# Kernel optimization log

Hardware: AMD Instinct MI355X
Metric: run time of the kernel (lower is better)

## Reference

```python
import jax, jax.numpy as jnp
import numpy as np

B, L = 2, 2048
D_MODEL = 512
KERNEL = 5
DILATIONS = (1, 2, 4, 8, 1, 2, 4, 8)
HEADS = len(DILATIONS)
HEAD_W = D_MODEL // HEADS
MODE = "center"


def _dilocal_content(x_bedl, kernel, dilations, mode):
    # x_bedl: (B, E, D, L). Returns content in layout (B, L, E, H, K, D),
    # matching LCSA's dilocal + transpose(-4,-1).transpose(-4,-2).transpose(-5,-4).
    Lx = x_bedl.shape[-1]
    per_head = []
    for d in dilations:
        P = (kernel - 1) * d
        if mode == "forward":
            pads = (P, 0)
        elif mode == "backward":
            pads = (0, P)
        else:  # center
            pads = (P // 2, P - P // 2)
        padded = jnp.pad(x_bedl, ((0, 0),) * (x_bedl.ndim - 1) + (pads,))
        win = jnp.stack([padded[..., k * d:k * d + Lx] for k in range(kernel)], axis=-2)
        per_head.append(win)
    c = jnp.stack(per_head, axis=-2)  # (B, E, D, K, H, L)
    return jnp.transpose(c, (0, 5, 1, 4, 3, 2))  # (B, L, E, H, K, D)


def setup_inputs() -> dict:
    key = jax.random.key(0)
    ks = jax.random.split(key, 6)
    s_in = 1.0 / np.sqrt(D_MODEL)
    s_out = 1.0 / np.sqrt(HEADS * HEAD_W)
    x = jax.random.normal(ks[0], (B, L, D_MODEL), jnp.float32)
    q_w = jax.random.normal(ks[1], (1, HEADS, 1, HEAD_W, D_MODEL), jnp.float32) * s_in
    q_b = jnp.zeros((1, HEADS, 1, HEAD_W), jnp.float32)
    k_w = jax.random.normal(ks[2], (1, HEADS, KERNEL, HEAD_W, D_MODEL), jnp.float32) * s_in
    k_b = jnp.zeros((1, HEADS, KERNEL, HEAD_W), jnp.float32)
    v_w = jax.random.normal(ks[3], (1, HEADS, KERNEL, HEAD_W, D_MODEL), jnp.float32) * s_in
    v_b = jnp.zeros((1, HEADS, KERNEL, HEAD_W), jnp.float32)
    o_w = jax.random.normal(ks[4], (1, D_MODEL, HEADS * HEAD_W), jnp.float32) * s_out
    o_b = jnp.zeros((1, D_MODEL), jnp.float32)
    return {"x": x, "q_w": q_w, "q_b": q_b, "k_w": k_w, "k_b": k_b,
            "v_w": v_w, "v_b": v_b, "o_w": o_w, "o_b": o_b}


def reference(x, q_w, q_b, k_w, k_b, v_w, v_b, o_w, o_b) -> jnp.ndarray:
    b, l, _ = x.shape
    # ensemble=None path: unsqueeze(-3) then transpose(-2,-1) -> (B, E=1, D, L)
    t = jnp.swapaxes(x[:, None, :, :], -2, -1)
    content = _dilocal_content(t, KERNEL, DILATIONS, MODE)  # (B, L, 1, H, K, D)
    # query uses kernel_width=1 (no padding, dilation irrelevant): (B, L, 1, H, 1, D)
    query = jnp.broadcast_to(x[:, :, None, None, None, :], (b, l, 1, HEADS, 1, D_MODEL))
    # per-(head, kernel-position) projections
    q = jnp.einsum('blehkd,ehkod->blehko', query, q_w) + q_b      # (B,L,1,H,1,O)
    k = jnp.einsum('blehkd,ehkod->blehko', content, k_w) + k_b    # (B,L,1,H,K,O)
    v = jnp.einsum('blehkd,ehkod->blehko', content, v_w) + v_b    # (B,L,1,H,K,O)
    logits = jnp.einsum('blehqo,blehko->blehqk', q, k)            # (B,L,1,H,1,K)
    score = jax.nn.softmax(logits, axis=-1)
    attn = jnp.einsum('blehqk,blehko->blehqo', score, v) / jnp.sqrt(jnp.float32(HEAD_W))
    attn = attn[..., 0, :]                                        # squeeze(-2) -> (B,L,1,H,O)
    flat = attn.reshape(b, l, 1, HEADS * HEAD_W)
    out = jnp.einsum('blef,eof->bleo', flat, o_w) + o_b           # (B,L,1,D)
    # transpose(-3,-2) then squeeze ensemble -> (B, L, D)
    return out[:, :, 0, :]
```

## Files before the change

kernel.cpp:

```cpp
#include <hip/hip_runtime.h>
#include <hip/hip_bf16.h>

using bf16 = __hip_bfloat16;
typedef __attribute__((ext_vector_type(8))) short short8;
typedef __attribute__((ext_vector_type(4))) float f32x4;

__device__ __constant__ int c_dil[8] = {1, 2, 4, 8, 1, 2, 4, 8};

__device__ inline void store1(float* p, float v) { *p = v; }
__device__ inline void store1(bf16* p, float v) { *p = __float2bfloat16(v); }

__device__ inline void gload_lds16(const void* g, void* l) {
    __builtin_amdgcn_global_load_lds(
        (const __attribute__((address_space(1))) unsigned int*)g,
        (__attribute__((address_space(3))) unsigned int*)l, 16, 0, 0);
}

template <int N> __device__ inline void vwait() {
    asm volatile("s_waitcnt vmcnt(%0)" :: "n"(N) : "memory");
    __builtin_amdgcn_sched_barrier(0);
}
__device__ inline void barrier_pin() {
    __builtin_amdgcn_s_barrier();
    __builtin_amdgcn_sched_barrier(0);
}

__device__ inline unsigned short f2bf(float f) {
    const unsigned u = __float_as_uint(f);
    return (unsigned short)((u + 0x7fffu + ((u >> 16) & 1u)) >> 16);
}
__device__ inline float bf2f(unsigned short h) { return __uint_as_float(((unsigned)h) << 16); }

__device__ inline void conv_block(const float* __restrict__ src, bf16* __restrict__ dst,
                                  int ld, int mode, int idx) {
    const float4 v = *reinterpret_cast<const float4*>(src + idx);
    const int r = idx >> 9, c = idx & 511;
    bf16* d = dst + (size_t)r * ld + c;
    const float vv[4] = {v.x, v.y, v.z, v.w};
    ushort4 hi, lo;
    unsigned short* hp = &hi.x; unsigned short* lp = &lo.x;
#pragma unroll
    for (int j = 0; j < 4; ++j) {
        hp[j] = f2bf(vv[j]);
        lp[j] = f2bf(vv[j] - bf2f(hp[j]));
    }
    *reinterpret_cast<ushort4*>(d) = hi;
    if (mode == 1) *reinterpret_cast<ushort4*>(d + 512) = lo;
}

__global__ __launch_bounds__(256) void conv_all(
    const float* __restrict__ x,  const float* __restrict__ qw, const float* __restrict__ kw,
    const float* __restrict__ vw, const float* __restrict__ ow,
    const float* __restrict__ qb, const float* __restrict__ kb,
    bf16* A2, bf16* Wqk, bf16* Wv, bf16* Wo, float* bqk)
{
    const int b = blockIdx.x, t = threadIdx.x;
    if (b < 2048)       conv_block(x,  A2,                      1024, 1, (b * 256 + t) * 4);
    else if (b < 2304)  conv_block(qw, Wqk,                      512, 0, ((b - 2048) * 256 + t) * 4);
    else if (b < 3584)  conv_block(kw, Wqk + (size_t)512 * 512,  512, 0, ((b - 2304) * 256 + t) * 4);
    else if (b < 4864)  conv_block(vw, Wv,                       512, 0, ((b - 3584) * 256 + t) * 4);
    else if (b < 5120)  conv_block(ow, Wo,                       512, 0, ((b - 4864) * 256 + t) * 4);
    else { const int i = (b - 5120) * 256 + t; bqk[i] = (i < 512) ? qb[i] : kb[i - 512]; }
}

template <bool HILO>
__device__ __forceinline__ void run_gemm(
    short* smem,
    const bf16* __restrict__ A,
    const bf16* __restrict__ W,
    const float* __restrict__ bias,
    bf16* __restrict__ C, int ldc,
    int bm, int bn)
{
    constexpr int NSTEPS = 16;
    short* Ahi = smem;
    short* Alo = smem + 8192;
    short* Bs  = smem + 16384;

    const int tid = threadIdx.x, wid = tid >> 6, lane = tid & 63;

    const int sslot = (((tid & 3) ^ ((tid >> 3) & 3)) << 4);
    const char* pAh = (const char*)A + (size_t)(bm + (tid >> 2)) * 2048 + sslot;
    const char* pB0 = (const char*)W + (size_t)(bn + (tid >> 2)) * 1024 + sslot;

    auto stage = [&](int kt) {
        char* da = (char*)(Ahi + (kt & 1) * 4096);
        char* db = (char*)(Bs  + (kt & 1) * 8192);
        gload_lds16(pAh,          da + wid * 1024);
        gload_lds16(pAh + 131072, da + 4096 + wid * 1024);
        if (HILO) {
            char* dl = (char*)(Alo + (kt & 1) * 4096);
            gload_lds16(pAh + 1024,          dl + wid * 1024);
            gload_lds16(pAh + 1024 + 131072, dl + 4096 + wid * 1024);
        }
        gload_lds16(pB0,           db + wid * 1024);
        gload_lds16(pB0 + 65536,   db + 4096 + wid * 1024);
        gload_lds16(pB0 + 131072,  db + 8192 + wid * 1024);
        gload_lds16(pB0 + 196608,  db + 12288 + wid * 1024);
        pAh += 64; pB0 += 64;
    };

    f32x4 acc[4][8];
#pragma unroll
    for (int m = 0; m < 4; ++m)
#pragma unroll
        for (int n = 0; n < 8; ++n) acc[m][n] = f32x4{0.f, 0.f, 0.f, 0.f};

    const int lr16 = lane & 15;
    const int koff = (((lane >> 4) ^ ((lr16 >> 1) & 3)) << 3);
    const int wrM = wid >> 1, wcN = wid & 1;
    const int arow0 = wrM * 64 + lr16;
    const int brow0 = wcN * 128 + lr16;

    stage(0);

    for (int kt = 0; kt < NSTEPS; ++kt) {
        vwait<0>();
        barrier_pin();

        const short* ah = Ahi + (kt & 1) * 4096;
        const short* al = Alo + (kt & 1) * 4096;
        const short* bb = Bs  + (kt & 1) * 8192;
        short8 fh[4], fl[4], bw[8];
#pragma unroll
        for (int m = 0; m < 4; ++m) {
            fh[m] = *(const short8*)&ah[(arow0 + m * 16) * 32 + koff];
            if (HILO) fl[m] = *(const short8*)&al[(arow0 + m * 16) * 32 + koff];
        }
#pragma unroll
        for (int n = 0; n < 8; ++n)
            bw[n] = *(const short8*)&bb[(brow0 + n * 16) * 32 + koff];

        if (kt + 1 < NSTEPS) stage(kt + 1);

        __builtin_amdgcn_s_setprio(1);
#pragma unroll
        for (int m = 0; m < 4; ++m)
#pragma unroll
            for (int n = 0; n < 8; ++n)
                acc[m][n] = __builtin_amdgcn_mfma_f32_16x16x32_bf16(fh[m], bw[n], acc[m][n], 0, 0, 0);
        if (HILO) {
#pragma unroll
            for (int m = 0; m < 4; ++m)
#pragma unroll
                for (int n = 0; n < 8; ++n)
                    acc[m][n] = __builtin_amdgcn_mfma_f32_16x16x32_bf16(fl[m], bw[n], acc[m][n], 0, 0, 0);
        }
        __builtin_amdgcn_s_setprio(0);
    }

    const int r4 = (lane >> 4) * 4;
#pragma unroll
    for (int m = 0; m < 4; ++m) {
#pragma unroll
        for (int n = 0; n < 8; ++n) {
            const int col = bn + wcN * 128 + n * 16 + lr16;
            const float bv = bias[col];
#pragma unroll
            for (int jj = 0; jj < 4; ++jj) {
                const int row = bm + wrM * 64 + m * 16 + r4 + jj;
                store1(C + (size_t)row * ldc + col, acc[m][n][jj] + bv);
            }
        }
    }
}

__global__ __launch_bounds__(256, 2) void gemm_qkv(
    const bf16* __restrict__ A,
    const bf16* __restrict__ Wqk, const float* __restrict__ bqk, bf16* __restrict__ PQK,
    const bf16* __restrict__ Wv,  const float* __restrict__ vb,  bf16* __restrict__ PV)
{
    __shared__ short smem[32768];
    const int b = blockIdx.x;
    if (b < 384) {
        const int xcd = b & 7, i = b >> 3;
        const int by = xcd * 4 + (i & 3), bx = i >> 2;
        run_gemm<true>(smem, A, Wqk, bqk, PQK, 3072, by * 128, bx * 256);
    } else {
        const int v = b - 384;
        const int xcd = v & 7, i = v >> 3;
        const int by = xcd * 4 + (i & 3), bx = i >> 2;
        run_gemm<false>(smem, A, Wv, vb, PV, 2560, by * 128, bx * 256);
    }
}

template <int BN, typename TC>
__global__ __launch_bounds__(256) void gemm128(
    const bf16* __restrict__ A, int lda, int cw, int rpx,
    const bf16* __restrict__ W0, int ldw0, const float* __restrict__ b0,
    TC* __restrict__ C0, int ldc0, int nt0, int nx0)
{
    constexpr int NF = BN / 32;
    constexpr int NLOAD = (BN == 128) ? 4 : 3;
    __shared__ short As[4][128 * 32];
    __shared__ short Bs[4][BN * 32];

    const int tid = threadIdx.x, wid = tid >> 6, lane = tid & 63;

    const int xcd = (int)blockIdx.x & 7;
    const int i   = (int)blockIdx.x >> 3;
    const int grp = rpx * cw;
    const int cc = i / grp, w2 = i % grp;
    const int rr = w2 / cw, c = w2 % cw;
    const int bx = cc * cw + c;
    const int by = xcd * rpx + rr;

    const int bm = by * 128;
    const int bn = bx * BN;
    const int nsteps = nt0;

    const int srow = lane >> 2;
    const int ssw  = (((lane & 3) ^ ((lane >> 3) & 3)) << 4);
    const char* pA0 = (const char*)A + (size_t)(bm + wid * 16 + srow) * lda * 2 + ssw;
    const char* pA1 = pA0 + (size_t)64 * lda * 2;
    const char* pB0 = (const char*)W0 + (size_t)(bn + wid * 16 + srow) * ldw0 * 2 + ssw;

    f32x4 acc[4][NF];
#pragma unroll
    for (int m = 0; m < 4; ++m)
#pragma unroll
        for (int n = 0; n < NF; ++n) acc[m][n] = f32x4{0.f, 0.f, 0.f, 0.f};

    const int lr16 = lane & 15;
    const int wsw8 = (((lane >> 4) ^ ((lr16 >> 1) & 3)) << 3);
    const int wr = wid >> 1, wc = wid & 1;
    int offA[4], offB[NF];
#pragma unroll
    for (int m = 0; m < 4; ++m) offA[m] = (wr * 4 + m) * 512 + lr16 * 32 + wsw8;
#pragma unroll
    for (int n = 0; n < NF; ++n) offB[n] = (wc * NF + n) * 512 + lr16 * 32 + wsw8;

    auto stage = [&](int buf) {
        gload_lds16(pA0, (char*)As[buf] + wid * 1024);
        gload_lds16(pA1, (char*)As[buf] + (wid + 4) * 1024);
        gload_lds16(pB0, (char*)Bs[buf] + wid * 1024);
        pA0 += 64; pA1 += 64; pB0 += 64;
    };

    stage(0);
    stage(1);
    stage(2);

    for (int s = 0; s < nsteps; ++s) {
        const int cur = s & 3;
        if (s + 2 < nsteps)      vwait<2 * NLOAD>();
        else if (s + 1 < nsteps) vwait<NLOAD>();
        else                     vwait<0>();
        barrier_pin();

        if (s + 3 < nsteps) stage((s + 3) & 3);

        short8 af[4], bw[NF];
#pragma unroll
        for (int m = 0; m < 4; ++m)
            af[m] = *(const short8*)&As[cur][offA[m]];
#pragma unroll
        for (int n = 0; n < NF; ++n)
            bw[n] = *(const short8*)&Bs[cur][offB[n]];

        __builtin_amdgcn_s_setprio(1);
#pragma unroll
        for (int m = 0; m < 4; ++m)
#pragma unroll
            for (int n = 0; n < NF; ++n)
                acc[m][n] = __builtin_amdgcn_mfma_f32_16x16x32_bf16(af[m], bw[n], acc[m][n], 0, 0, 0);
        __builtin_amdgcn_s_setprio(0);
    }

    const int r4 = (lane >> 4) * 4;
#pragma unroll
    for (int m = 0; m < 4; ++m) {
#pragma unroll
        for (int n = 0; n < NF; ++n) {
            const int col = bn + wc * (NF * 16) + n * 16 + lr16;
            const float bv = b0[col];
#pragma unroll
            for (int jj = 0; jj < 4; ++jj) {
                const int row = bm + wr * 64 + m * 16 + r4 + jj;
                store1(C0 + (size_t)row * ldc0 + col, acc[m][n][jj] + bv);
            }
        }
    }
}

__global__ __launch_bounds__(256) void attn_k(
    const bf16* __restrict__ PQK, const bf16* __restrict__ PV, bf16* __restrict__ Aout)
{
    const int lane = threadIdx.x & 63;
    const int wave = threadIdx.x >> 6;
    const int bl = blockIdx.x * 4 + wave;
    const int l  = bl & 2047;
    const int h  = lane >> 3;
    const int d  = c_dil[h];
    const int o8 = (lane & 7) * 8;

    float q[8];
    {
        const short8 qv = *(const short8*)&PQK[(size_t)bl * 3072 + lane * 8];
#pragma unroll
        for (int i = 0; i < 8; ++i) q[i] = bf2f((unsigned short)qv[i]);
    }

    float logits[5];
    float vv[5][8];
#pragma unroll
    for (int kk = 0; kk < 5; ++kk) {
        const int pos = l + (kk - 2) * d;
        const bool ok = (pos >= 0) && (pos < 2048);
        float s = 0.f;
        if (ok) {
            const size_t rb = (size_t)(bl - l + pos);
            const int coff = h * 320 + kk * 64 + o8;
            const short8 kv = *(const short8*)&PQK[rb * 3072 + 512 + coff];
            const short8 vvv = *(const short8*)&PV[rb * 2560 + coff];
#pragma unroll
            for (int i = 0; i < 8; ++i) {
                s = fmaf(bf2f((unsigned short)kv[i]), q[i], s);
                vv[kk][i] = bf2f((unsigned short)vvv[i]);
            }
        } else {
#pragma unroll
            for (int i = 0; i < 8; ++i) vv[kk][i] = 0.f;
        }
        s += __shfl_xor(s, 1);
        s += __shfl_xor(s, 2);
        s += __shfl_xor(s, 4);
        logits[kk] = s;
    }

    float mx = logits[0];
#pragma unroll
    for (int kk = 1; kk < 5; ++kk) mx = fmaxf(mx, logits[kk]);
    float e[5], ssum = 0.f;
#pragma unroll
    for (int kk = 0; kk < 5; ++kk) { e[kk] = __expf(logits[kk] - mx); ssum += e[kk]; }
    const float sc = 0.125f / ssum;

    short8 outv;
#pragma unroll
    for (int i = 0; i < 8; ++i) {
        float a = 0.f;
#pragma unroll
        for (int kk = 0; kk < 5; ++kk) a = fmaf(e[kk], vv[kk][i], a);
        outv[i] = (short)f2bf(a * sc);
    }
    *(short8*)&Aout[(size_t)bl * 512 + lane * 8] = outv;
}

extern "C" void kernel_launch(void* const* d_in, const int* in_sizes, int n_in,
                              void* d_out, int out_size, void* d_ws, size_t ws_size,
                              hipStream_t stream)
{
    const float* x   = (const float*)d_in[0];
    const float* q_w = (const float*)d_in[1];
    const float* q_b = (const float*)d_in[2];
    const float* k_w = (const float*)d_in[3];
    const float* k_b = (const float*)d_in[4];
    const float* v_w = (const float*)d_in[5];
    const float* v_b = (const float*)d_in[6];
    const float* o_w = (const float*)d_in[7];
    const float* o_b = (const float*)d_in[8];
    float* out = (float*)d_out;

    const int M = 4096;

    char* p = (char*)d_ws;
    bf16* A2  = (bf16*)p;  p += (size_t)M * 1024 * 2;
    bf16* Wqk = (bf16*)p;  p += (size_t)3072 * 512 * 2;
    bf16* Wv  = (bf16*)p;  p += (size_t)2560 * 512 * 2;
    bf16* Wo  = (bf16*)p;  p += (size_t)512 * 512 * 2;
    float* bqk = (float*)p; p += 3072 * 4;
    bf16* PQK = (bf16*)p;  p += (size_t)M * 3072 * 2;
    bf16* PV  = (bf16*)p;
    bf16* Aout = A2;

    conv_all<<<dim3(5132), dim3(256), 0, stream>>>(x, q_w, k_w, v_w, o_w, q_b, k_b,
                                                   A2, Wqk, Wv, Wo, bqk);
    gemm_qkv<<<dim3(704), dim3(256), 0, stream>>>(A2, Wqk, bqk, PQK, Wv, v_b, PV);
    attn_k<<<dim3(2048), dim3(256), 0, stream>>>(PQK, PV, Aout);
    gemm128<64, float><<<dim3(256), dim3(256), 0, stream>>>(
        Aout, 512, 8, 4,
        Wo, 512, o_b, out, 512, 16, 8);
}
```

Measured before the change: 76.05 us.

## Load GEMM operand fragments directly from global memory instead of LDS staging

```diff
diff --git a/kernel.cpp b/kernel.cpp
--- a/kernel.cpp
+++ b/kernel.cpp
@@ -65,7 +65,6 @@
 
 template <bool HILO>
 __device__ __forceinline__ void run_gemm(
-    short* smem,
     const bf16* __restrict__ A,
     const bf16* __restrict__ W,
     const float* __restrict__ bias,
@@ -73,32 +72,14 @@
     int bm, int bn)
 {
     constexpr int NSTEPS = 16;
-    short* Ahi = smem;
-    short* Alo = smem + 8192;
-    short* Bs  = smem + 16384;
-
     const int tid = threadIdx.x, wid = tid >> 6, lane = tid & 63;
 
-    const int sslot = (((tid & 3) ^ ((tid >> 3) & 3)) << 4);
-    const char* pAh = (const char*)A + (size_t)(bm + (tid >> 2)) * 2048 + sslot;
-    const char* pB0 = (const char*)W + (size_t)(bn + (tid >> 2)) * 1024 + sslot;
-
-    auto stage = [&](int kt) {
-        char* da = (char*)(Ahi + (kt & 1) * 4096);
-        char* db = (char*)(Bs  + (kt & 1) * 8192);
-        gload_lds16(pAh,          da + wid * 1024);
-        gload_lds16(pAh + 131072, da + 4096 + wid * 1024);
-        if (HILO) {
-            char* dl = (char*)(Alo + (kt & 1) * 4096);
-            gload_lds16(pAh + 1024,          dl + wid * 1024);
-            gload_lds16(pAh + 1024 + 131072, dl + 4096 + wid * 1024);
-        }
-        gload_lds16(pB0,           db + wid * 1024);
-        gload_lds16(pB0 + 65536,   db + 4096 + wid * 1024);
-        gload_lds16(pB0 + 131072,  db + 8192 + wid * 1024);
-        gload_lds16(pB0 + 196608,  db + 12288 + wid * 1024);
-        pAh += 64; pB0 += 64;
-    };
+    const int lr16 = lane & 15;
+    const int hi8  = (lane >> 4) * 8;
+    const int wrM = wid >> 1, wcN = wid & 1;
+
+    const bf16* Abase = A + (size_t)(bm + wrM * 64 + lr16) * 1024;
+    const bf16* Bbase = W + (size_t)(bn + wcN * 128 + lr16) * 512;
 
     f32x4 acc[4][8];
 #pragma unroll
@@ -106,32 +87,18 @@
 #pragma unroll
         for (int n = 0; n < 8; ++n) acc[m][n] = f32x4{0.f, 0.f, 0.f, 0.f};
 
-    const int lr16 = lane & 15;
-    const int koff = (((lane >> 4) ^ ((lr16 >> 1) & 3)) << 3);
-    const int wrM = wid >> 1, wcN = wid & 1;
-    const int arow0 = wrM * 64 + lr16;
-    const int brow0 = wcN * 128 + lr16;
-
-    stage(0);
-
+#pragma unroll 2
     for (int kt = 0; kt < NSTEPS; ++kt) {
-        vwait<0>();
-        barrier_pin();
-
-        const short* ah = Ahi + (kt & 1) * 4096;
-        const short* al = Alo + (kt & 1) * 4096;
-        const short* bb = Bs  + (kt & 1) * 8192;
+        const int kc = kt * 32 + hi8;
         short8 fh[4], fl[4], bw[8];
 #pragma unroll
         for (int m = 0; m < 4; ++m) {
-            fh[m] = *(const short8*)&ah[(arow0 + m * 16) * 32 + koff];
-            if (HILO) fl[m] = *(const short8*)&al[(arow0 + m * 16) * 32 + koff];
+            fh[m] = *(const short8*)&Abase[(size_t)(m * 16) * 1024 + kc];
+            if (HILO) fl[m] = *(const short8*)&Abase[(size_t)(m * 16) * 1024 + 512 + kc];
         }
 #pragma unroll
         for (int n = 0; n < 8; ++n)
-            bw[n] = *(const short8*)&bb[(brow0 + n * 16) * 32 + koff];
-
-        if (kt + 1 < NSTEPS) stage(kt + 1);
+            bw[n] = *(const short8*)&Bbase[(size_t)(n * 16) * 512 + kc];
 
         __builtin_amdgcn_s_setprio(1);
 #pragma unroll
@@ -170,17 +137,16 @@
     const bf16* __restrict__ Wqk, const float* __restrict__ bqk, bf16* __restrict__ PQK,
     const bf16* __restrict__ Wv,  const float* __restrict__ vb,  bf16* __restrict__ PV)
 {
-    __shared__ short smem[32768];
     const int b = blockIdx.x;
     if (b < 384) {
         const int xcd = b & 7, i = b >> 3;
         const int by = xcd * 4 + (i & 3), bx = i >> 2;
-        run_gemm<true>(smem, A, Wqk, bqk, PQK, 3072, by * 128, bx * 256);
+        run_gemm<true>(A, Wqk, bqk, PQK, 3072, by * 128, bx * 256);
     } else {
         const int v = b - 384;
         const int xcd = v & 7, i = v >> 3;
         const int by = xcd * 4 + (i & 3), bx = i >> 2;
-        run_gemm<false>(smem, A, Wv, vb, PV, 2560, by * 128, bx * 256);
+        run_gemm<false>(A, Wv, vb, PV, 2560, by * 128, bx * 256);
     }
 }
 
```

Measured after the change: 122.6 us. 1.61x slower.
